# Kernel optimization log

Hardware: AMD Instinct MI355X
Metric: run time of the kernel (lower is better)

Reference implementation:

```python
import jax, jax.numpy as jnp
import numpy as np

D = 1024
H = 16
K = D // H
B = 2
S = 2048

def setup_inputs() -> dict:
    key = jax.random.key(0)
    k1, k2, k3, k4, k5 = jax.random.split(key, 5)
    x = jax.random.normal(k1, (B, S, D), dtype=jnp.float32)
    # nn.Linear(d, 3d): weight [3d, d], bias [3d]
    Wqkv = jax.random.normal(k2, (3 * D, D), dtype=jnp.float32) / np.sqrt(D)
    bqkv = jax.random.normal(k3, (3 * D,), dtype=jnp.float32) * 0.01
    Wproj = jax.random.normal(k4, (D, D), dtype=jnp.float32) / np.sqrt(D)
    bproj = jax.random.normal(k5, (D,), dtype=jnp.float32) * 0.01
    return {"x": x, "Wqkv": Wqkv, "bqkv": bqkv, "Wproj": Wproj, "bproj": bproj}

def reference(x, Wqkv, bqkv, Wproj, bproj):
    Bsz, Slen, d = x.shape
    # fused QKV projection: [B,S,3d] -> [B,S,3,H,K] -> (3, B, H, S, K)
    qkv = (jnp.einsum('bsd,ed->bse', x, Wqkv) + bqkv).reshape(Bsz, Slen, 3, H, K)
    q, k, v = jnp.moveaxis(qkv, 2, 0).transpose(0, 1, 3, 2, 4)
    scale = 1.0 / jnp.sqrt(jnp.asarray(K, dtype=x.dtype))
    scores = jnp.einsum('bhqk,bhmk->bhqm', q, k) * scale  # [B,H,S,S]
    a = jax.nn.softmax(scores, axis=-1)
    # dropout is identity in eval mode
    o = jnp.einsum('bhqm,bhmk->bhqk', a, v)  # [B,H,S,K]
    o = o.transpose(0, 2, 1, 3).reshape(Bsz, Slen, d)
    return jnp.einsum('bsd,ed->bse', o, Wproj) + bproj
```

## Files before the change

kernel.cpp:

```cpp
#include <hip/hip_runtime.h>
#include <cstdint>

typedef unsigned short ushort_t;
typedef short short8 __attribute__((ext_vector_type(8)));
typedef float f32x4 __attribute__((ext_vector_type(4)));
typedef float float4v __attribute__((ext_vector_type(4)));
typedef unsigned int uint2v __attribute__((ext_vector_type(2)));
typedef unsigned int uint4v __attribute__((ext_vector_type(4)));

#define DDIM 1024
#define HH 16
#define HEADK 64
#define BB 2
#define SS 2048

#if __has_builtin(__builtin_amdgcn_exp2f)
#define EXP2F(x) __builtin_amdgcn_exp2f(x)
#else
#define EXP2F(x) exp2f(x)
#endif

__device__ __forceinline__ ushort_t f2bf(float f) {
  union { float f; uint32_t u; } c; c.f = f;
  uint32_t u = c.u;
  u += 0x7fffu + ((u >> 16) & 1u);
  return (ushort_t)(u >> 16);
}

__device__ __forceinline__ uint32_t pkbf_trunc(float a, float b) {
  union { float f; uint32_t u; } ca, cb;
  ca.f = a; cb.f = b;
  return __builtin_amdgcn_perm(cb.u, ca.u, 0x07060302);
}

__device__ __forceinline__ uint32_t pkbf_rne(float a, float b) {
  return (uint32_t)f2bf(a) | ((uint32_t)f2bf(b) << 16);
}

__device__ __forceinline__ float bfhi2f(uint32_t u) {
  union { uint32_t u; float f; } c; c.u = u & 0xffff0000u; return c.f;
}
__device__ __forceinline__ float bflo2f(uint32_t u) {
  union { uint32_t u; float f; } c; c.u = u << 16; return c.f;
}

__device__ __forceinline__ void glds16(const ushort_t* gp, ushort_t* lp) {
  __builtin_amdgcn_global_load_lds(
      (const __attribute__((address_space(1))) uint32_t*)gp,
      (__attribute__((address_space(3))) uint32_t*)lp, 16, 0, 0);
}

__global__ void cvt3_kernel(const float* __restrict__ s0, ushort_t* __restrict__ d0, int n0,
                            const float* __restrict__ s1, ushort_t* __restrict__ d1, int n1,
                            const float* __restrict__ s2, ushort_t* __restrict__ d2, int n2) {
  int i = blockIdx.x * blockDim.x + threadIdx.x;
  const float* src; ushort_t* dst; int k;
  if (i < n0) { src = s0; dst = d0; k = i; }
  else if (i < n0 + n1) { src = s1; dst = d1; k = i - n0; }
  else if (i < n0 + n1 + n2) { src = s2; dst = d2; k = i - n0 - n1; }
  else return;
  float4v v = ((const float4v*)src)[k];
  uint2v o; o[0] = pkbf_rne(v[0], v[1]); o[1] = pkbf_rne(v[2], v[3]);
  ((uint2v*)dst)[k] = o;
}

__global__ __launch_bounds__(256) void gemm_qkv128(
    const ushort_t* __restrict__ A, const ushort_t* __restrict__ Bm,
    const float* __restrict__ bias, ushort_t* __restrict__ Cbf) {
  constexpr int Kd = 1024;
  __shared__ ushort_t smem[128 * 64 * 2];
  ushort_t* As = smem;
  ushort_t* Bs = smem + 128 * 64;
  const int tid = threadIdx.x;
  const int wv = tid >> 6, lane = tid & 63;
  const int l15 = lane & 15, quad = lane >> 4;
  const int wm = wv >> 1, wn = wv & 1;

  const int lin = blockIdx.x + 24 * blockIdx.y;
  const int xcd = lin & 7, g = lin >> 3;
  const int by = xcd + 8 * (g & 3);
  const int bx = g >> 2;
  const int tm0 = by * 128, tn0 = bx * 128;

  f32x4 acc[4][4];
#pragma unroll
  for (int i = 0; i < 4; ++i)
#pragma unroll
    for (int j = 0; j < 4; ++j) acc[i][j] = (f32x4){0.f, 0.f, 0.f, 0.f};

  const int lrow = lane >> 3;
  const int gcb = (lane & 7) ^ lrow;

  for (int k0 = 0; k0 < Kd; k0 += 64) {
#pragma unroll
    for (int c = 0; c < 4; ++c) {
      int seg = wv * 4 + c;
      glds16(A + (size_t)(tm0 + seg * 8 + lrow) * Kd + k0 + gcb * 8,
             As + seg * 512);
    }
#pragma unroll
    for (int c = 0; c < 4; ++c) {
      int seg = wv * 4 + c;
      glds16(Bm + (size_t)(tn0 + seg * 8 + lrow) * Kd + k0 + gcb * 8,
             Bs + seg * 512);
    }
    __syncthreads();
#pragma unroll
    for (int kk = 0; kk < 64; kk += 32) {
      short8 af[4], bfr[4];
#pragma unroll
      for (int i = 0; i < 4; ++i) {
        int r = wm * 64 + i * 16 + l15;
        int cb = (kk >> 3) + quad;
        af[i] = *(const short8*)(As + r * 64 + ((cb ^ (l15 & 7)) << 3));
      }
#pragma unroll
      for (int j = 0; j < 4; ++j) {
        int r = wn * 64 + j * 16 + l15;
        int cb = (kk >> 3) + quad;
        bfr[j] = *(const short8*)(Bs + r * 64 + ((cb ^ (l15 & 7)) << 3));
      }
#pragma unroll
      for (int i = 0; i < 4; ++i)
#pragma unroll
        for (int j = 0; j < 4; ++j)
          acc[i][j] = __builtin_amdgcn_mfma_f32_16x16x32_bf16(
              af[i], bfr[j], acc[i][j], 0, 0, 0);
    }
    __syncthreads();
  }

  const int t = tn0 >> 10;
  if (t < 2) {
#pragma unroll
    for (int j = 0; j < 4; ++j) {
      int col = tn0 + wn * 64 + j * 16 + l15;
      float bv = bias[col];
      int hh = (col >> 6) & 15, kk2 = col & 63;
#pragma unroll
      for (int i = 0; i < 4; ++i) {
        int row0 = tm0 + wm * 64 + i * 16 + quad * 4;
#pragma unroll
        for (int r = 0; r < 4; ++r) {
          int row = row0 + r;
          int b = row >> 11, s = row & 2047;
          float v = acc[i][j][r] + bv;
          if (t == 0) v *= 0.18033688f;
          size_t base = (((size_t)t * BB + b) * HH + hh) * ((size_t)SS * HEADK);
          Cbf[base + (size_t)s * HEADK + kk2] = f2bf(v);
        }
      }
    }
  } else {
    __syncthreads();
#pragma unroll
    for (int j = 0; j < 4; ++j) {
      int c = wn * 64 + j * 16 + l15;
      float bv = bias[tn0 + c];
#pragma unroll
      for (int i = 0; i < 4; ++i) {
        int row0 = wm * 64 + i * 16 + quad * 4;
        uint2v dw;
        dw[0] = pkbf_rne(acc[i][j][0] + bv, acc[i][j][1] + bv);
        dw[1] = pkbf_rne(acc[i][j][2] + bv, acc[i][j][3] + bv);
        int rb = row0 >> 3;
        *(uint2v*)(&smem[c * 128 + (((rb ^ (c & 15)) << 3) | (row0 & 7))]) = dw;
      }
    }
    __syncthreads();
    const int rb2 = lane & 15;
    const int cg = lane >> 4;
#pragma unroll
    for (int it = 0; it < 8; ++it) {
      int c = wv * 32 + it * 4 + cg;
      short8 vv = *(const short8*)(&smem[c * 128 + ((rb2 ^ (c & 15)) << 3)]);
      int gcol = tn0 + c;
      int hh = (gcol >> 6) & 15, kk2 = gcol & 63;
      int grow = tm0 + rb2 * 8;
      int b = grow >> 11, s = grow & 2047;
      size_t base = (((size_t)2 * BB + b) * HH + hh) * ((size_t)SS * HEADK);
      *(short8*)(&Cbf[base + (size_t)kk2 * SS + s]) = vv;
    }
  }
}

__global__ __launch_bounds__(256, 2) void gemm_proj(
    const ushort_t* __restrict__ Op0, const ushort_t* __restrict__ Op1,
    const float* __restrict__ Lp, const ushort_t* __restrict__ Bm,
    const float* __restrict__ bias, float* __restrict__ Cout) {
  constexpr int Kd = 1024;
  constexpr size_t nsL = (size_t)BB * HH * SS;
  __shared__ ushort_t smem[2 * 12288];
  const int tid = threadIdx.x;
  const int wv = tid >> 6, lane = tid & 63;
  const int l15 = lane & 15, quad = lane >> 4;
  const int wm = wv >> 1, wn = wv & 1;
  const int lrow = lane >> 3, gcb = (lane & 7) ^ lrow;

  const int lin = blockIdx.x + 16 * blockIdx.y;
  const int xcd = lin & 7, g = lin >> 3;
  const int by = xcd + 8 * (g & 3);
  const int bx = g >> 2;
  const int tm0 = by * 128, tn0 = bx * 64;

  f32x4 acc[4][2];
#pragma unroll
  for (int i = 0; i < 4; ++i)
#pragma unroll
    for (int j = 0; j < 2; ++j) acc[i][j] = (f32x4){0.f, 0.f, 0.f, 0.f};

  uint4v ra0[2], ra1[2], rb0[2], rb1[2];
  float rl0[2], rl1[2];

  auto readA = [&](int t) {
#pragma unroll
    for (int c = 0; c < 2; ++c) {
      int u = tid + 256 * c;
      int row = u >> 2, cg = u & 3;
      int grow = tm0 + row;
      int ab = grow >> 11, as_ = grow & 2047;
      size_t lo = (size_t)(ab * HH + t) * SS + as_;
      size_t po = lo * 64 + cg * 16;
      ra0[c] = *(const uint4v*)(Op0 + po);
      ra1[c] = *(const uint4v*)(Op0 + po + 8);
      rb0[c] = *(const uint4v*)(Op1 + po);
      rb1[c] = *(const uint4v*)(Op1 + po + 8);
      rl0[c] = Lp[lo];
      rl1[c] = Lp[nsL + lo];
    }
  };
  auto writeA = [&](int p) {
    ushort_t* As = smem + p * 12288;
#pragma unroll
    for (int c = 0; c < 2; ++c) {
      int u = tid + 256 * c;
      int row = u >> 2, cg = u & 3;
      float inv = 1.0f / (rl0[c] + rl1[c]);
      uint4v olo, ohi;
#pragma unroll
      for (int d = 0; d < 4; ++d) {
        olo[d] = pkbf_rne((bflo2f(ra0[c][d]) + bflo2f(rb0[c][d])) * inv,
                          (bfhi2f(ra0[c][d]) + bfhi2f(rb0[c][d])) * inv);
        ohi[d] = pkbf_rne((bflo2f(ra1[c][d]) + bflo2f(rb1[c][d])) * inv,
                          (bfhi2f(ra1[c][d]) + bfhi2f(rb1[c][d])) * inv);
      }
      *(uint4v*)(&As[row * 64 + (((cg * 2) ^ (row & 7)) << 3)]) = olo;
      *(uint4v*)(&As[row * 64 + (((cg * 2 + 1) ^ (row & 7)) << 3)]) = ohi;
    }
  };
  auto stageB = [&](int t, int p) {
    ushort_t* Bs = smem + p * 12288 + 8192;
#pragma unroll
    for (int c = 0; c < 2; ++c) {
      int seg = wv * 2 + c;
      glds16(Bm + (size_t)(tn0 + seg * 8 + lrow) * Kd + t * 64 + gcb * 8,
             Bs + seg * 512);
    }
  };

  readA(0);
  __builtin_amdgcn_sched_barrier(0);
  stageB(0, 0);
  __builtin_amdgcn_sched_barrier(0);
  asm volatile("s_waitcnt vmcnt(2)" ::: "memory");
  writeA(0);

  for (int t = 0; t < 16; ++t) {
    const int p = t & 1;
    asm volatile("s_waitcnt lgkmcnt(0)" ::: "memory");
    __builtin_amdgcn_s_barrier();
    __builtin_amdgcn_sched_barrier(0);
    if (t + 1 < 16) {
      readA(t + 1);
      __builtin_amdgcn_sched_barrier(0);
      stageB(t + 1, p ^ 1);
      __builtin_amdgcn_sched_barrier(0);
      asm volatile("s_waitcnt vmcnt(14)" ::: "memory");
    } else {
      asm volatile("s_waitcnt vmcnt(0)" ::: "memory");
    }
    __builtin_amdgcn_s_barrier();
    asm volatile("" ::: "memory");
    __builtin_amdgcn_sched_barrier(0);

    const ushort_t* As = smem + p * 12288;
    const ushort_t* Bs = As + 8192;
    short8 bfr[2][2], af[4][2];
#pragma unroll
    for (int j = 0; j < 2; ++j)
#pragma unroll
      for (int kc = 0; kc < 2; ++kc) {
        int n = wn * 32 + j * 16 + l15;
        bfr[j][kc] =
            *(const short8*)(Bs + n * 64 + (((kc * 4 + quad) ^ (l15 & 7)) << 3));
      }
#pragma unroll
    for (int mi = 0; mi < 4; ++mi)
#pragma unroll
      for (int kc = 0; kc < 2; ++kc) {
        int r = wm * 64 + mi * 16 + l15;
        af[mi][kc] =
            *(const short8*)(As + r * 64 + (((kc * 4 + quad) ^ (l15 & 7)) << 3));
      }
    __builtin_amdgcn_s_setprio(1);
#pragma unroll
    for (int kc = 0; kc < 2; ++kc)
#pragma unroll
      for (int mi = 0; mi < 4; ++mi)
#pragma unroll
        for (int j = 0; j < 2; ++j)
          acc[mi][j] = __builtin_amdgcn_mfma_f32_16x16x32_bf16(
              af[mi][kc], bfr[j][kc], acc[mi][j], 0, 0, 0);
    __builtin_amdgcn_s_setprio(0);

    if (t + 1 < 16) writeA(p ^ 1);
  }

#pragma unroll
  for (int j = 0; j < 2; ++j) {
    int col = tn0 + wn * 32 + j * 16 + l15;
    float bv = bias[col];
#pragma unroll
    for (int mi = 0; mi < 4; ++mi) {
      int row0 = tm0 + wm * 64 + mi * 16 + quad * 4;
#pragma unroll
      for (int r = 0; r < 4; ++r)
        Cout[(size_t)(row0 + r) * 1024 + col] = acc[mi][j][r] + bv;
    }
  }
}

template <int NSPLIT>
__global__ __launch_bounds__(256, 4) void attn_kernel(
    const ushort_t* __restrict__ qkv, ushort_t* __restrict__ O0,
    ushort_t* __restrict__ O1, float* __restrict__ Lp) {
  constexpr int NT = (SS / NSPLIT) / 32;
  __shared__ ushort_t Kt[3][32 * 64];
  __shared__ ushort_t Vt[3][64 * 32];
  __shared__ ushort_t Pw[4][2][32 * 32];

  const int lin = blockIdx.x + 16 * (blockIdx.y + 16 * blockIdx.z);
  const int xcd = lin & 7, ii = lin >> 3;
  const int qt = ii & 15;
  const int hz = (ii >> 4) * 8 + xcd;
  const int h = hz & 15;
  const int z = hz >> 4;
  const int b = z >> 1, ns = z & 1;
  const int tid = threadIdx.x;
  const int wv = tid >> 6, lane = tid & 63;
  const int l15 = lane & 15, quad = lane >> 4;

  const size_t hstride = (size_t)SS * HEADK;
  const ushort_t* Qg = qkv + ((size_t)(0 * BB + b) * HH + h) * hstride;
  const ushort_t* Kg = qkv + ((size_t)(1 * BB + b) * HH + h) * hstride;
  const ushort_t* Vg = qkv + ((size_t)(2 * BB + b) * HH + h) * hstride;
  ushort_t* Opp = ns ? O1 : O0;

  short8 qf[2][2];
#pragma unroll
  for (int mi = 0; mi < 2; ++mi)
#pragma unroll
    for (int kc = 0; kc < 2; ++kc)
      qf[mi][kc] = *(const short8*)(
          Qg + (size_t)(qt * 128 + wv * 32 + mi * 16 + l15) * 64 + kc * 32 +
          quad * 8);

  const short ONE = (short)0x3F80;
  short8 ones = {ONE, ONE, ONE, ONE, ONE, ONE, ONE, ONE};

  f32x4 oat[2][4];
  f32x4 loa[2];
#pragma unroll
  for (int mi = 0; mi < 2; ++mi) {
    loa[mi] = (f32x4){0.f, 0.f, 0.f, 0.f};
#pragma unroll
    for (int c = 0; c < 4; ++c) oat[mi][c] = (f32x4){0.f, 0.f, 0.f, 0.f};
  }

  const int lrow = lane >> 3, gcb = (lane & 7) ^ lrow;
  const int vfl = lane >> 2;
  const int vgb = (lane & 3) ^ ((vfl >> 1) & 3);

  const int pos0 = ns * (SS / NSPLIT);

  auto stage = [&](int jj, int db) {
    glds16(Kg + (size_t)(pos0 + jj * 32 + wv * 8 + lrow) * 64 + gcb * 8,
           &Kt[db][wv * 512]);
    glds16(Vg + (size_t)(wv * 16 + vfl) * SS + pos0 + jj * 32 + vgb * 8,
           &Vt[db][wv * 512]);
  };

  auto qk_phase = [&](int kb, int pb) {
    f32x4 st[2][2];
    __builtin_amdgcn_s_setprio(1);
#pragma unroll
    for (int cf = 0; cf < 2; ++cf) {
      int n = cf * 16 + l15;
      short8 kf0 = *(const short8*)(&Kt[kb][n * 64 + ((quad ^ (n & 7)) << 3)]);
      short8 kf1 =
          *(const short8*)(&Kt[kb][n * 64 + (((quad + 4) ^ (n & 7)) << 3)]);
#pragma unroll
      for (int mi = 0; mi < 2; ++mi) {
        f32x4 z2 = (f32x4){0.f, 0.f, 0.f, 0.f};
        z2 = __builtin_amdgcn_mfma_f32_16x16x32_bf16(kf0, qf[mi][0], z2, 0, 0, 0);
        z2 = __builtin_amdgcn_mfma_f32_16x16x32_bf16(kf1, qf[mi][1], z2, 0, 0, 0);
        st[mi][cf] = z2;
      }
    }
    __builtin_amdgcn_s_setprio(0);
#pragma unroll
    for (int mi = 0; mi < 2; ++mi)
#pragma unroll
      for (int cf = 0; cf < 2; ++cf) {
        float e0 = EXP2F(st[mi][cf][0]);
        float e1 = EXP2F(st[mi][cf][1]);
        float e2 = EXP2F(st[mi][cf][2]);
        float e3 = EXP2F(st[mi][cf][3]);
        uint2v dw;
        dw[0] = pkbf_trunc(e0, e1);
        dw[1] = pkbf_trunc(e2, e3);
        int row = mi * 16 + l15;
        int pbv = 2 * cf + (quad >> 1);
        int pbs = pbv ^ ((l15 >> 1) & 3);
        *(uint2v*)(&Pw[wv][pb][row * 32 + pbs * 8 + (quad & 1) * 4]) = dw;
      }
  };

  stage(0, 0);
  stage(1, 1);

  asm volatile("s_waitcnt vmcnt(2)" ::: "memory");
  __builtin_amdgcn_s_barrier();
  asm volatile("" ::: "memory");
  __builtin_amdgcn_sched_barrier(0);
  qk_phase(0, 0);

  int vb = 0;
  for (int j = 0; j < NT; ++j) {
    const int kb = (vb == 2) ? 0 : vb + 1;
    const int sb = (kb == 2) ? 0 : kb + 1;
    asm volatile("s_waitcnt vmcnt(0)" ::: "memory");
    __builtin_amdgcn_s_barrier();
    asm volatile("" ::: "memory");
    __builtin_amdgcn_sched_barrier(0);

    if (j + 2 < NT) stage(j + 2, sb);
    if (j + 1 < NT) qk_phase(kb, (j + 1) & 1);

    short8 pa[2];
#pragma unroll
    for (int mi = 0; mi < 2; ++mi) {
      int row = mi * 16 + l15;
      pa[mi] = *(const short8*)(&Pw[wv][j & 1][row * 32 +
                                              ((quad ^ ((l15 >> 1) & 3)) << 3)]);
    }
    __builtin_amdgcn_s_setprio(1);
#pragma unroll
    for (int cf = 0; cf < 4; ++cf) {
      short8 vf = *(const short8*)(&Vt[vb][(cf * 16 + l15) * 32 +
                                           ((quad ^ ((l15 >> 1) & 3)) << 3)]);
#pragma unroll
      for (int mi = 0; mi < 2; ++mi)
        oat[mi][cf] = __builtin_amdgcn_mfma_f32_16x16x32_bf16(
            vf, pa[mi], oat[mi][cf], 0, 0, 0);
    }
#pragma unroll
    for (int mi = 0; mi < 2; ++mi)
      loa[mi] = __builtin_amdgcn_mfma_f32_16x16x32_bf16(ones, pa[mi], loa[mi],
                                                        0, 0, 0);
    __builtin_amdgcn_s_setprio(0);

    vb = kb;
  }

  const size_t obase = ((size_t)b * HH + h) * SS * HEADK;
#pragma unroll
  for (int mi = 0; mi < 2; ++mi) {
#pragma unroll
    for (int cf = 0; cf < 4; ++cf) {
      uint2v dw;
      dw[0] = pkbf_rne(oat[mi][cf][0], oat[mi][cf][1]);
      dw[1] = pkbf_rne(oat[mi][cf][2], oat[mi][cf][3]);
      int cb = 2 * cf + (quad >> 1);
      int cbs = cb ^ (l15 & 7);
      *(uint2v*)(&Pw[wv][0][l15 * 64 + cbs * 8 + (quad & 1) * 4]) = dw;
    }
    const int r = lane >> 2;
#pragma unroll
    for (int pass = 0; pass < 2; ++pass) {
      int g = (lane & 3) + 4 * pass;
      short8 ov = *(const short8*)(&Pw[wv][0][r * 64 + ((g ^ (r & 7)) << 3)]);
      int qrow = qt * 128 + wv * 32 + mi * 16 + r;
      *(short8*)(&Opp[obase + (size_t)qrow * 64 + g * 8]) = ov;
    }
    if (quad == 0) {
      int qrow = qt * 128 + wv * 32 + mi * 16 + l15;
      Lp[((size_t)(ns * BB + b) * HH + h) * SS + qrow] = loa[mi][0];
    }
  }
}

extern "C" void kernel_launch(void* const* d_in, const int* in_sizes, int n_in,
                              void* d_out, int out_size, void* d_ws,
                              size_t ws_size, hipStream_t stream) {
  const float* x = (const float*)d_in[0];
  const float* Wqkv = (const float*)d_in[1];
  const float* bqkv = (const float*)d_in[2];
  const float* Wproj = (const float*)d_in[3];
  const float* bproj = (const float*)d_in[4];
  float* out = (float*)d_out;

  ushort_t* xb = (ushort_t*)d_ws;
  ushort_t* wqb = xb + (size_t)4096 * 1024;
  ushort_t* wpb = wqb + (size_t)3072 * 1024;
  ushort_t* qkvb = wpb + (size_t)1024 * 1024;
  ushort_t* Op1 = qkvb + (size_t)3 * BB * HH * SS * HEADK;
  ushort_t* Op0 = xb;
  float* Lp = (float*)wqb;

  const int n0 = 4096 * 1024 / 4, n1 = 3072 * 1024 / 4, n2 = 1024 * 1024 / 4;
  cvt3_kernel<<<(n0 + n1 + n2 + 255) / 256, 256, 0, stream>>>(
      x, xb, n0, Wqkv, wqb, n1, Wproj, wpb, n2);
  gemm_qkv128<<<dim3(3072 / 128, 4096 / 128), 256, 0, stream>>>(xb, wqb, bqkv,
                                                                qkvb);
  attn_kernel<2><<<dim3(16, 16, 4), 256, 0, stream>>>(qkvb, Op0, Op1, Lp);
  gemm_proj<<<dim3(1024 / 64, 4096 / 128), 256, 0, stream>>>(
      Op0, Op1, Lp, wpb, bproj, out);
}
```

Measured before the change: 191.8 us.

## Deepen A-operand prefetch in output projection to two tiles ahead

Adds a second register set so the global loads and combination of the split-attention partial outputs for the projection GEMM are issued two K-steps ahead instead of one. The synchronization is restructured with a single barrier per iteration and explicit vmcnt waits, and the loop is fully unrolled so the register set chosen each step is resolved at compile time. The aim is to hide global-load latency behind the MFMA work. It costs extra VGPRs, which may reduce occupancy under the 4-wave launch bound, and the hand-counted vmcnt values must match the actual number of outstanding loads to stay correct.

```diff
diff --git a/kernel.cpp b/kernel.cpp
--- a/kernel.cpp
+++ b/kernel.cpp
@@ -209,47 +209,50 @@
 #pragma unroll
     for (int j = 0; j < 2; ++j) acc[i][j] = (f32x4){0.f, 0.f, 0.f, 0.f};
 
-  uint4v ra0[2], ra1[2], rb0[2], rb1[2];
-  float rl0[2], rl1[2];
-
-  auto readA = [&](int t) {
+  struct ARegs {
+    uint4v ra0[2], ra1[2], rb0[2], rb1[2];
+    float rl0[2], rl1[2];
+  };
+  ARegs sA, sB;
+
+  auto readA = [&](int t, ARegs& S) {
 #pragma unroll
     for (int c = 0; c < 2; ++c) {
       int u = tid + 256 * c;
       int row = u >> 2, cg = u & 3;
-      int grow = tm0 + row;
-      int ab = grow >> 11, as_ = grow & 2047;
+      int grw = tm0 + row;
+      int ab = grw >> 11, as_ = grw & 2047;
       size_t lo = (size_t)(ab * HH + t) * SS + as_;
       size_t po = lo * 64 + cg * 16;
-      ra0[c] = *(const uint4v*)(Op0 + po);
-      ra1[c] = *(const uint4v*)(Op0 + po + 8);
-      rb0[c] = *(const uint4v*)(Op1 + po);
-      rb1[c] = *(const uint4v*)(Op1 + po + 8);
-      rl0[c] = Lp[lo];
-      rl1[c] = Lp[nsL + lo];
+      S.ra0[c] = *(const uint4v*)(Op0 + po);
+      S.ra1[c] = *(const uint4v*)(Op0 + po + 8);
+      S.rb0[c] = *(const uint4v*)(Op1 + po);
+      S.rb1[c] = *(const uint4v*)(Op1 + po + 8);
+      S.rl0[c] = Lp[lo];
+      S.rl1[c] = Lp[nsL + lo];
     }
   };
-  auto writeA = [&](int p) {
-    ushort_t* As = smem + p * 12288;
+  auto writeA = [&](const ARegs& S, int pp) {
+    ushort_t* As = smem + pp * 12288;
 #pragma unroll
     for (int c = 0; c < 2; ++c) {
       int u = tid + 256 * c;
       int row = u >> 2, cg = u & 3;
-      float inv = 1.0f / (rl0[c] + rl1[c]);
+      float inv = 1.0f / (S.rl0[c] + S.rl1[c]);
       uint4v olo, ohi;
 #pragma unroll
       for (int d = 0; d < 4; ++d) {
-        olo[d] = pkbf_rne((bflo2f(ra0[c][d]) + bflo2f(rb0[c][d])) * inv,
-                          (bfhi2f(ra0[c][d]) + bfhi2f(rb0[c][d])) * inv);
-        ohi[d] = pkbf_rne((bflo2f(ra1[c][d]) + bflo2f(rb1[c][d])) * inv,
-                          (bfhi2f(ra1[c][d]) + bfhi2f(rb1[c][d])) * inv);
+        olo[d] = pkbf_rne((bflo2f(S.ra0[c][d]) + bflo2f(S.rb0[c][d])) * inv,
+                          (bfhi2f(S.ra0[c][d]) + bfhi2f(S.rb0[c][d])) * inv);
+        ohi[d] = pkbf_rne((bflo2f(S.ra1[c][d]) + bflo2f(S.rb1[c][d])) * inv,
+                          (bfhi2f(S.ra1[c][d]) + bfhi2f(S.rb1[c][d])) * inv);
       }
       *(uint4v*)(&As[row * 64 + (((cg * 2) ^ (row & 7)) << 3)]) = olo;
       *(uint4v*)(&As[row * 64 + (((cg * 2 + 1) ^ (row & 7)) << 3)]) = ohi;
     }
   };
-  auto stageB = [&](int t, int p) {
-    ushort_t* Bs = smem + p * 12288 + 8192;
+  auto stageB = [&](int t, int pp) {
+    ushort_t* Bs = smem + pp * 12288 + 8192;
 #pragma unroll
     for (int c = 0; c < 2; ++c) {
       int seg = wv * 2 + c;
@@ -258,30 +261,30 @@
     }
   };
 
-  readA(0);
+  readA(0, sA);
   __builtin_amdgcn_sched_barrier(0);
   stageB(0, 0);
   __builtin_amdgcn_sched_barrier(0);
-  asm volatile("s_waitcnt vmcnt(2)" ::: "memory");
-  writeA(0);
-
+  readA(1, sB);
+  __builtin_amdgcn_sched_barrier(0);
+  asm volatile("s_waitcnt vmcnt(14)" ::: "memory");
+  writeA(sA, 0);
+  asm volatile("s_waitcnt lgkmcnt(0)" ::: "memory");
+  asm volatile("s_waitcnt vmcnt(12)" ::: "memory");
+  __builtin_amdgcn_s_barrier();
+  __builtin_amdgcn_sched_barrier(0);
+
+#pragma unroll
   for (int t = 0; t < 16; ++t) {
     const int p = t & 1;
-    asm volatile("s_waitcnt lgkmcnt(0)" ::: "memory");
-    __builtin_amdgcn_s_barrier();
-    __builtin_amdgcn_sched_barrier(0);
     if (t + 1 < 16) {
-      readA(t + 1);
-      __builtin_amdgcn_sched_barrier(0);
       stageB(t + 1, p ^ 1);
       __builtin_amdgcn_sched_barrier(0);
-      asm volatile("s_waitcnt vmcnt(14)" ::: "memory");
-    } else {
-      asm volatile("s_waitcnt vmcnt(0)" ::: "memory");
-    }
-    __builtin_amdgcn_s_barrier();
-    asm volatile("" ::: "memory");
-    __builtin_amdgcn_sched_barrier(0);
+    }
+    if (t + 2 < 16) {
+      if (t & 1) readA(t + 2, sB); else readA(t + 2, sA);
+      __builtin_amdgcn_sched_barrier(0);
+    }
 
     const ushort_t* As = smem + p * 12288;
     const ushort_t* Bs = As + 8192;
@@ -313,7 +316,20 @@
               af[mi][kc], bfr[j][kc], acc[mi][j], 0, 0, 0);
     __builtin_amdgcn_s_setprio(0);
 
-    if (t + 1 < 16) writeA(p ^ 1);
+    if (t + 1 < 16) {
+      if (t < 14)
+        asm volatile("s_waitcnt vmcnt(14)" ::: "memory");
+      else
+        asm volatile("s_waitcnt vmcnt(2)" ::: "memory");
+      if (t & 1) writeA(sA, p ^ 1); else writeA(sB, p ^ 1);
+      asm volatile("s_waitcnt lgkmcnt(0)" ::: "memory");
+      if (t < 14)
+        asm volatile("s_waitcnt vmcnt(12)" ::: "memory");
+      else
+        asm volatile("s_waitcnt vmcnt(0)" ::: "memory");
+      __builtin_amdgcn_s_barrier();
+      __builtin_amdgcn_sched_barrier(0);
+    }
   }
 
 #pragma unroll
```

Result: no change. 192.9 us (median of 2 runs) (+0.6%).
